# Optimization experiments

Hardware: AMD Instinct MI355X
Metric: run time of the kernel (lower is better)

## Reference

```python
import jax, jax.numpy as jnp
import numpy as np

MB, NUM, LENTH, SIZE, OUT = 16, 128, 64, 256, 256
DIN = (LENTH + 1) * 2  # aux_lenth = 0


def setup_inputs() -> dict:
    key = jax.random.key(0)
    ks = jax.random.split(key, 9)
    s = 0.05
    return {
        "in_": jax.random.normal(ks[0], (MB, NUM, LENTH), dtype=jnp.float32),
        "W1": jax.random.normal(ks[1], (DIN, SIZE), dtype=jnp.float32) * s,
        "b1": jax.random.normal(ks[2], (SIZE,), dtype=jnp.float32) * s,
        "W2": jax.random.normal(ks[3], (SIZE, SIZE), dtype=jnp.float32) * s,
        "b2": jax.random.normal(ks[4], (SIZE,), dtype=jnp.float32) * s,
        "W3": jax.random.normal(ks[5], (SIZE, SIZE), dtype=jnp.float32) * s,
        "b3": jax.random.normal(ks[6], (SIZE,), dtype=jnp.float32) * s,
        "W4": jax.random.normal(ks[7], (SIZE, OUT), dtype=jnp.float32) * s,
        "b4": jax.random.normal(ks[8], (OUT,), dtype=jnp.float32) * s,
    }


def reference(in_, W1, b1, W2, b2, W3, b3, W4, b4):
    mb, num, _ = in_.shape
    # append coordinate channel: coord[i] = i  -> [mb, num, lenth+1]
    coord = jnp.broadcast_to(
        jnp.arange(num, dtype=in_.dtype)[None, :, None], (mb, num, 1)
    )
    x = jnp.concatenate([in_, coord], axis=2)  # [mb, num, L1], L1 = lenth+1
    L1 = x.shape[2]
    # pairwise: x_full[b, a, j] = concat(x[b, j], x[b, a])
    x_i = jnp.broadcast_to(x[:, None, :, :], (mb, num, num, L1))  # varies over j
    x_j = jnp.broadcast_to(x[:, :, None, :], (mb, num, num, L1))  # varies over a
    x_full = jnp.concatenate([x_i, x_j], axis=3)  # [mb, num, num, 2*L1]
    h = x_full.reshape(mb * num * num, 2 * L1)
    h = jax.nn.relu(h @ W1 + b1)
    h = jax.nn.relu(h @ W2 + b2)
    h = jax.nn.relu(h @ W3 + b3)
    h = jax.nn.relu(h @ W4 + b4)  # [mb*num*num, OUT]
    x_g = h.reshape(mb, num * num, -1).sum(axis=1)  # [mb, OUT]
    return x_g
```

## Files before the change

kernel.cpp:

```cpp
#include <hip/hip_runtime.h>
#include <hip/hip_bf16.h>

using short8 = __attribute__((ext_vector_type(8))) short;
using f32x4  = __attribute__((ext_vector_type(4))) float;

#define MBATCH 16
#define NUMV   128
#define LEN    64
#define SZ     256

__device__ __forceinline__ unsigned short bfbits(float x) {
  union { float f; unsigned u; } c; c.f = x;
  return (unsigned short)((c.u + 0x8000u) >> 16);
}

__global__ void uv_prep(const float* __restrict__ in_, const float* __restrict__ W1,
                        const float* __restrict__ b1,
                        float* __restrict__ u, float* __restrict__ v) {
  int bn = blockIdx.x;
  int n  = bn & (NUMV - 1);
  int s  = threadIdx.x;
  __shared__ float xs[LEN];
  if (s < LEN) xs[s] = in_[bn * LEN + s];
  __syncthreads();
  float fn = (float)n;
  float uu = fn * W1[64 * SZ + s];
  float vv = fn * W1[129 * SZ + s] + b1[s];
  for (int c = 0; c < LEN; ++c) {
    uu = fmaf(xs[c], W1[c * SZ + s], uu);
    vv = fmaf(xs[c], W1[(65 + c) * SZ + s], vv);
  }
  u[bn * SZ + s] = uu;
  v[bn * SZ + s] = vv;
}

__global__ void w_prep(const float* __restrict__ W2, const float* __restrict__ W3,
                       const float* __restrict__ W4, short* __restrict__ wlay) {
  int L = blockIdx.x >> 3, kb = blockIdx.x & 7;
  const float* W = (L == 0) ? W2 : (L == 1) ? W3 : W4;
  int m = threadIdx.x >> 6, lane = threadIdx.x & 63;
  int l16 = lane & 15, q = lane >> 4;
  for (int wv = 0; wv < 4; ++wv) {
    int ch = wv * 64 + m * 16 + l16;
    short8 pk;
    for (int i = 0; i < 8; ++i)
      pk[i] = (short)bfbits(W[(kb * 32 + q * 8 + i) * SZ + ch]);
    int f = ((L * 4 + wv) * 4 + m) * 8 + kb;
    reinterpret_cast<short8*>(wlay)[f * 64 + lane] = pk;
  }
}

__global__ __launch_bounds__(256, 2) void fused_mlp(
    const float* __restrict__ u, const float* __restrict__ v,
    const short* __restrict__ wlay,
    const float* __restrict__ b2, const float* __restrict__ b3, const float* __restrict__ b4,
    float* __restrict__ partial) {
  __shared__ __align__(16) short hbuf[64 * 256];

  int wg = blockIdx.x;
  int b = wg >> 8, a = (wg >> 1) & 127, jh = wg & 1;
  int tid = threadIdx.x;
  int wave = tid >> 6, lane = tid & 63;
  int l16 = lane & 15, q = lane >> 4;

  const short8* wcl = reinterpret_cast<const short8*>(wlay) + lane;

  short8 awA[4], awB[4];
  #pragma unroll
  for (int m = 0; m < 4; ++m)
    awA[m] = wcl[(((0 * 4 + wave) * 4 + m) * 8 + 0) * 64];

  {
    const float4* ub = (const float4*)(u + (size_t)b * NUMV * SZ) + jh * 64 * 64;
    const float4* vb = (const float4*)(v + ((size_t)b * NUMV + a) * SZ);
    #pragma unroll
    for (int it = 0; it < 16; ++it) {
      int flat = tid + it * 256;
      int jr = flat >> 6, c4 = flat & 63;
      float4 uu = ub[jr * 64 + c4];
      float4 vv = vb[c4];
      unsigned lo = (unsigned)bfbits(fmaxf(uu.x + vv.x, 0.f))
                  | ((unsigned)bfbits(fmaxf(uu.y + vv.y, 0.f)) << 16);
      unsigned hi = (unsigned)bfbits(fmaxf(uu.z + vv.z, 0.f))
                  | ((unsigned)bfbits(fmaxf(uu.w + vv.w, 0.f)) << 16);
      int byte = (jr * 512 + c4 * 8) ^ ((jr & 7) << 4);
      uint2 pk; pk.x = lo; pk.y = hi;
      *reinterpret_cast<uint2*>((char*)hbuf + byte) = pk;
    }
  }

  __syncthreads();

  #pragma unroll
  for (int L = 0; L < 3; ++L) {
    const float* bb = (L == 0) ? b2 : (L == 1) ? b3 : b4;

    f32x4 acc[4][4];
    #pragma unroll
    for (int m = 0; m < 4; ++m)
      #pragma unroll
      for (int n = 0; n < 4; ++n)
        acc[m][n] = f32x4{0.f, 0.f, 0.f, 0.f};

    #pragma unroll
    for (int kb = 0; kb < 8; ++kb) {
      if (kb < 7) {
        if ((kb & 1) == 0) {
          #pragma unroll
          for (int m = 0; m < 4; ++m)
            awB[m] = wcl[(((L * 4 + wave) * 4 + m) * 8 + kb + 1) * 64];
        } else {
          #pragma unroll
          for (int m = 0; m < 4; ++m)
            awA[m] = wcl[(((L * 4 + wave) * 4 + m) * 8 + kb + 1) * 64];
        }
      } else if (L < 2) {
        #pragma unroll
        for (int m = 0; m < 4; ++m)
          awA[m] = wcl[((((L + 1) * 4 + wave) * 4 + m) * 8 + 0) * 64];
      }
      short8 bfr[4];
      #pragma unroll
      for (int n = 0; n < 4; ++n) {
        int row = n * 16 + l16;
        int byte = (row * 512 + kb * 64 + q * 16) ^ ((row & 7) << 4);
        bfr[n] = *reinterpret_cast<const short8*>((char*)hbuf + byte);
      }
      __builtin_amdgcn_s_setprio(1);
      if ((kb & 1) == 0) {
        #pragma unroll
        for (int m = 0; m < 4; ++m)
          #pragma unroll
          for (int n = 0; n < 4; ++n)
            acc[m][n] = __builtin_amdgcn_mfma_f32_16x16x32_bf16(awA[m], bfr[n], acc[m][n], 0, 0, 0);
      } else {
        #pragma unroll
        for (int m = 0; m < 4; ++m)
          #pragma unroll
          for (int n = 0; n < 4; ++n)
            acc[m][n] = __builtin_amdgcn_mfma_f32_16x16x32_bf16(awB[m], bfr[n], acc[m][n], 0, 0, 0);
      }
      __builtin_amdgcn_s_setprio(0);
    }

    __syncthreads();

    if (L < 2) {
      #pragma unroll
      for (int m = 0; m < 4; ++m) {
        f32x4 bv = *reinterpret_cast<const f32x4*>(bb + wave * 64 + m * 16 + q * 4);
        int ch = wave * 64 + m * 16 + q * 4;
        #pragma unroll
        for (int n = 0; n < 4; ++n) {
          int row = n * 16 + l16;
          f32x4 t = acc[m][n];
          unsigned lo = (unsigned)bfbits(fmaxf(t[0] + bv[0], 0.f))
                      | ((unsigned)bfbits(fmaxf(t[1] + bv[1], 0.f)) << 16);
          unsigned hi = (unsigned)bfbits(fmaxf(t[2] + bv[2], 0.f))
                      | ((unsigned)bfbits(fmaxf(t[3] + bv[3], 0.f)) << 16);
          int byte = (row * 512 + ch * 2) ^ ((row & 7) << 4);
          uint2 pk; pk.x = lo; pk.y = hi;
          *reinterpret_cast<uint2*>((char*)hbuf + byte) = pk;
        }
      }
      __syncthreads();
    } else {
      #pragma unroll
      for (int m = 0; m < 4; ++m) {
        f32x4 bv = *reinterpret_cast<const f32x4*>(bb + wave * 64 + m * 16 + q * 4);
        f32x4 s = f32x4{0.f, 0.f, 0.f, 0.f};
        #pragma unroll
        for (int n = 0; n < 4; ++n) {
          s[0] += fmaxf(acc[m][n][0] + bv[0], 0.f);
          s[1] += fmaxf(acc[m][n][1] + bv[1], 0.f);
          s[2] += fmaxf(acc[m][n][2] + bv[2], 0.f);
          s[3] += fmaxf(acc[m][n][3] + bv[3], 0.f);
        }
        #pragma unroll
        for (int r = 0; r < 4; ++r) {
          float x = s[r];
          x += __shfl_xor(x, 1);
          x += __shfl_xor(x, 2);
          x += __shfl_xor(x, 4);
          x += __shfl_xor(x, 8);
          s[r] = x;
        }
        if (l16 == 0) {
          float4 o; o.x = s[0]; o.y = s[1]; o.z = s[2]; o.w = s[3];
          *reinterpret_cast<float4*>(partial + (size_t)wg * SZ + wave * 64 + m * 16 + q * 4) = o;
        }
      }
    }
  }
}

__global__ void reduce_partials(const float* __restrict__ partial, float* __restrict__ out) {
  int b = blockIdx.x;
  int s = threadIdx.x;
  const float* p = partial + (size_t)b * 256 * SZ + s;
  float acc = 0.f;
  for (int i = 0; i < 256; ++i) acc += p[(size_t)i * SZ];
  out[b * SZ + s] = acc;
}

extern "C" void kernel_launch(void* const* d_in, const int* in_sizes, int n_in,
                              void* d_out, int out_size, void* d_ws, size_t ws_size,
                              hipStream_t stream) {
  const float* in_ = (const float*)d_in[0];
  const float* W1  = (const float*)d_in[1];
  const float* b1  = (const float*)d_in[2];
  const float* W2  = (const float*)d_in[3];
  const float* b2  = (const float*)d_in[4];
  const float* W3  = (const float*)d_in[5];
  const float* b3  = (const float*)d_in[6];
  const float* W4  = (const float*)d_in[7];
  const float* b4  = (const float*)d_in[8];
  float* out = (float*)d_out;

  char* ws = (char*)d_ws;
  float* u       = (float*)(ws);
  float* v       = (float*)(ws + (2u << 20));
  short* wlay    = (short*)(ws + (4u << 20));
  float* partial = (float*)(ws + (4u << 20) + (1u << 19));

  uv_prep<<<MBATCH * NUMV, 256, 0, stream>>>(in_, W1, b1, u, v);
  w_prep<<<24, 256, 0, stream>>>(W2, W3, W4, wlay);
  fused_mlp<<<MBATCH * NUMV * 2, 256, 0, stream>>>(u, v, wlay, b2, b3, b4, partial);
  reduce_partials<<<MBATCH, 256, 0, stream>>>(partial, out);
}
```

Measured before the change: 129.7 us.

## Enlarge fused MLP tile to 128 rows with 2x2 wave split and reorganized weights

Each workgroup now handles all 128 j rows for one (b,a) pair instead of 64, and its four waves are arranged as 2 row-halves by 2 channel-halves, each computing 8x4 MFMA tiles. The weight layout is reordered so the two waves sharing a channel half stream the same weight fragments, which halves weight traffic per output row and doubles MFMA work per weight load. The final per-row sums are combined through shared memory before writing, so the partial buffer and reduction shrink to 128 entries. It also removes the setprio hints. In exchange, LDS use doubles to 64KB and accumulator registers double, which may cut occupancy, and the grid is halved to 2048 workgroups.

```diff
diff --git a/kernel.cpp b/kernel.cpp
--- a/kernel.cpp
+++ b/kernel.cpp
@@ -38,15 +38,17 @@
                        const float* __restrict__ W4, short* __restrict__ wlay) {
   int L = blockIdx.x >> 3, kb = blockIdx.x & 7;
   const float* W = (L == 0) ? W2 : (L == 1) ? W3 : W4;
-  int m = threadIdx.x >> 6, lane = threadIdx.x & 63;
+  int mq = threadIdx.x >> 6, lane = threadIdx.x & 63;
   int l16 = lane & 15, q = lane >> 4;
   for (int wv = 0; wv < 4; ++wv) {
-    int ch = wv * 64 + m * 16 + l16;
+    int wch = wv >> 1, mhi = wv & 1;
+    int m = mhi * 4 + mq;
+    int ch = wch * 128 + m * 16 + l16;
     short8 pk;
     for (int i = 0; i < 8; ++i)
       pk[i] = (short)bfbits(W[(kb * 32 + q * 8 + i) * SZ + ch]);
-    int f = ((L * 4 + wv) * 4 + m) * 8 + kb;
-    reinterpret_cast<short8*>(wlay)[f * 64 + lane] = pk;
+    size_t byteoff = (size_t)(L * 8 + kb) * 16384 + wch * 8192 + m * 1024 + lane * 16;
+    *reinterpret_cast<short8*>((char*)wlay + byteoff) = pk;
   }
 }
 
@@ -55,26 +57,27 @@
     const short* __restrict__ wlay,
     const float* __restrict__ b2, const float* __restrict__ b3, const float* __restrict__ b4,
     float* __restrict__ partial) {
-  __shared__ __align__(16) short hbuf[64 * 256];
+  __shared__ __align__(16) short hbuf[128 * 256];
 
   int wg = blockIdx.x;
-  int b = wg >> 8, a = (wg >> 1) & 127, jh = wg & 1;
+  int b = wg >> 7, a = wg & 127;
   int tid = threadIdx.x;
   int wave = tid >> 6, lane = tid & 63;
+  int wch = wave & 1, wrow = wave >> 1;
   int l16 = lane & 15, q = lane >> 4;
 
-  const short8* wcl = reinterpret_cast<const short8*>(wlay) + lane;
-
-  short8 awA[4], awB[4];
+  const char* wptr = (const char*)wlay + wch * 8192 + lane * 16;
+
+  short8 awA[8], awB[8];
   #pragma unroll
-  for (int m = 0; m < 4; ++m)
-    awA[m] = wcl[(((0 * 4 + wave) * 4 + m) * 8 + 0) * 64];
+  for (int m = 0; m < 8; ++m)
+    awA[m] = *reinterpret_cast<const short8*>(wptr + m * 1024);
 
   {
-    const float4* ub = (const float4*)(u + (size_t)b * NUMV * SZ) + jh * 64 * 64;
+    const float4* ub = (const float4*)(u + (size_t)b * NUMV * SZ);
     const float4* vb = (const float4*)(v + ((size_t)b * NUMV + a) * SZ);
     #pragma unroll
-    for (int it = 0; it < 16; ++it) {
+    for (int it = 0; it < 32; ++it) {
       int flat = tid + it * 256;
       int jr = flat >> 6, c4 = flat & 63;
       float4 uu = ub[jr * 64 + c4];
@@ -95,64 +98,60 @@
   for (int L = 0; L < 3; ++L) {
     const float* bb = (L == 0) ? b2 : (L == 1) ? b3 : b4;
 
-    f32x4 acc[4][4];
+    f32x4 acc[8][4];
     #pragma unroll
-    for (int m = 0; m < 4; ++m)
+    for (int m = 0; m < 8; ++m)
       #pragma unroll
       for (int n = 0; n < 4; ++n)
         acc[m][n] = f32x4{0.f, 0.f, 0.f, 0.f};
 
     #pragma unroll
     for (int kb = 0; kb < 8; ++kb) {
-      if (kb < 7) {
+      if (L * 8 + kb < 23) {
         if ((kb & 1) == 0) {
           #pragma unroll
-          for (int m = 0; m < 4; ++m)
-            awB[m] = wcl[(((L * 4 + wave) * 4 + m) * 8 + kb + 1) * 64];
+          for (int m = 0; m < 8; ++m)
+            awB[m] = *reinterpret_cast<const short8*>(wptr + 16384 + m * 1024);
         } else {
           #pragma unroll
-          for (int m = 0; m < 4; ++m)
-            awA[m] = wcl[(((L * 4 + wave) * 4 + m) * 8 + kb + 1) * 64];
-        }
-      } else if (L < 2) {
-        #pragma unroll
-        for (int m = 0; m < 4; ++m)
-          awA[m] = wcl[((((L + 1) * 4 + wave) * 4 + m) * 8 + 0) * 64];
-      }
+          for (int m = 0; m < 8; ++m)
+            awA[m] = *reinterpret_cast<const short8*>(wptr + 16384 + m * 1024);
+        }
+      }
+      wptr += 16384;
+
       short8 bfr[4];
       #pragma unroll
       for (int n = 0; n < 4; ++n) {
-        int row = n * 16 + l16;
+        int row = wrow * 64 + n * 16 + l16;
         int byte = (row * 512 + kb * 64 + q * 16) ^ ((row & 7) << 4);
         bfr[n] = *reinterpret_cast<const short8*>((char*)hbuf + byte);
       }
-      __builtin_amdgcn_s_setprio(1);
       if ((kb & 1) == 0) {
         #pragma unroll
-        for (int m = 0; m < 4; ++m)
+        for (int m = 0; m < 8; ++m)
           #pragma unroll
           for (int n = 0; n < 4; ++n)
             acc[m][n] = __builtin_amdgcn_mfma_f32_16x16x32_bf16(awA[m], bfr[n], acc[m][n], 0, 0, 0);
       } else {
         #pragma unroll
-        for (int m = 0; m < 4; ++m)
+        for (int m = 0; m < 8; ++m)
           #pragma unroll
           for (int n = 0; n < 4; ++n)
             acc[m][n] = __builtin_amdgcn_mfma_f32_16x16x32_bf16(awB[m], bfr[n], acc[m][n], 0, 0, 0);
       }
-      __builtin_amdgcn_s_setprio(0);
     }
 
     __syncthreads();
 
     if (L < 2) {
       #pragma unroll
-      for (int m = 0; m < 4; ++m) {
-        f32x4 bv = *reinterpret_cast<const f32x4*>(bb + wave * 64 + m * 16 + q * 4);
-        int ch = wave * 64 + m * 16 + q * 4;
+      for (int m = 0; m < 8; ++m) {
+        int ch = wch * 128 + m * 16 + q * 4;
+        f32x4 bv = *reinterpret_cast<const f32x4*>(bb + ch);
         #pragma unroll
         for (int n = 0; n < 4; ++n) {
-          int row = n * 16 + l16;
+          int row = wrow * 64 + n * 16 + l16;
           f32x4 t = acc[m][n];
           unsigned lo = (unsigned)bfbits(fmaxf(t[0] + bv[0], 0.f))
                       | ((unsigned)bfbits(fmaxf(t[1] + bv[1], 0.f)) << 16);
@@ -165,9 +164,11 @@
       }
       __syncthreads();
     } else {
-      #pragma unroll
-      for (int m = 0; m < 4; ++m) {
-        f32x4 bv = *reinterpret_cast<const f32x4*>(bb + wave * 64 + m * 16 + q * 4);
+      float* pbuf = (float*)hbuf;
+      #pragma unroll
+      for (int m = 0; m < 8; ++m) {
+        int ch = wch * 128 + m * 16 + q * 4;
+        f32x4 bv = *reinterpret_cast<const f32x4*>(bb + ch);
         f32x4 s = f32x4{0.f, 0.f, 0.f, 0.f};
         #pragma unroll
         for (int n = 0; n < 4; ++n) {
@@ -187,9 +188,12 @@
         }
         if (l16 == 0) {
           float4 o; o.x = s[0]; o.y = s[1]; o.z = s[2]; o.w = s[3];
-          *reinterpret_cast<float4*>(partial + (size_t)wg * SZ + wave * 64 + m * 16 + q * 4) = o;
-        }
-      }
+          *reinterpret_cast<float4*>(pbuf + wrow * 256 + ch) = o;
+        }
+      }
+      __syncthreads();
+      if (tid < 256)
+        partial[(size_t)wg * SZ + tid] = pbuf[tid] + pbuf[256 + tid];
     }
   }
 }
@@ -197,9 +201,9 @@
 __global__ void reduce_partials(const float* __restrict__ partial, float* __restrict__ out) {
   int b = blockIdx.x;
   int s = threadIdx.x;
-  const float* p = partial + (size_t)b * 256 * SZ + s;
+  const float* p = partial + (size_t)b * NUMV * SZ + s;
   float acc = 0.f;
-  for (int i = 0; i < 256; ++i) acc += p[(size_t)i * SZ];
+  for (int i = 0; i < NUMV; ++i) acc += p[(size_t)i * SZ];
   out[b * SZ + s] = acc;
 }
 
@@ -225,6 +229,6 @@
 
   uv_prep<<<MBATCH * NUMV, 256, 0, stream>>>(in_, W1, b1, u, v);
   w_prep<<<24, 256, 0, stream>>>(W2, W3, W4, wlay);
-  fused_mlp<<<MBATCH * NUMV * 2, 256, 0, stream>>>(u, v, wlay, b2, b3, b4, partial);
+  fused_mlp<<<MBATCH * NUMV, 256, 0, stream>>>(u, v, wlay, b2, b3, b4, partial);
   reduce_partials<<<MBATCH, 256, 0, stream>>>(partial, out);
 }
```

Measured after the change: 136.6 us. 5.3% more time.
